# Performance work log

Measured on AMD Instinct MI355X. Metric: run time of the kernel, lower is better.

The kernel has to match this reference:

```python
import jax, jax.numpy as jnp
import numpy as np

INPUT_SIZE = 256
HIDDEN_SIZE = 256

def setup_inputs() -> dict:
    key = jax.random.key(0)
    ks = jax.random.split(key, 10)
    B = 65536
    scale_in = 1.0 / np.sqrt(INPUT_SIZE)
    scale_h = 1.0 / np.sqrt(HIDDEN_SIZE)
    inp = {
        "x": jax.random.normal(ks[0], (B, INPUT_SIZE), dtype=jnp.float32),
        "h_prev": jax.random.normal(ks[1], (B, HIDDEN_SIZE), dtype=jnp.float32),
        # nn.Linear weights are [out, in]; torch computes x @ W.T
        "W_z": jax.random.uniform(ks[2], (HIDDEN_SIZE, INPUT_SIZE), jnp.float32, -scale_in, scale_in),
        "U_z": jax.random.uniform(ks[3], (HIDDEN_SIZE, HIDDEN_SIZE), jnp.float32, -scale_h, scale_h),
        "b_z": jnp.zeros((HIDDEN_SIZE,), dtype=jnp.float32),
        "W_a": jax.random.uniform(ks[4], (HIDDEN_SIZE, INPUT_SIZE), jnp.float32, -scale_in, scale_in),
        "U_a": jax.random.uniform(ks[5], (HIDDEN_SIZE, HIDDEN_SIZE), jnp.float32, -scale_h, scale_h),
        "v_a": jax.random.normal(ks[6], (HIDDEN_SIZE,), dtype=jnp.float32),
        "W_h": jax.random.uniform(ks[7], (HIDDEN_SIZE, INPUT_SIZE), jnp.float32, -scale_in, scale_in),
        "U_h": jax.random.uniform(ks[8], (HIDDEN_SIZE, HIDDEN_SIZE), jnp.float32, -scale_h, scale_h),
        "b_h": jnp.zeros((HIDDEN_SIZE,), dtype=jnp.float32),
    }
    return inp

def reference(x, h_prev, W_z, U_z, b_z, W_a, U_a, v_a, W_h, U_h, b_h):
    # update gate
    z_t = jax.nn.sigmoid(x @ W_z.T + h_prev @ U_z.T + b_z)  # [B, H]
    # attention-based reset replacement
    attention_input = jnp.tanh(x @ W_a.T + h_prev @ U_a.T)   # [B, H]
    attention_weights = jax.nn.softmax(attention_input * v_a, axis=-1)
    attended_h = attention_weights * h_prev                   # [B, H]
    # candidate state
    h_tilde = jnp.tanh(x @ W_h.T + attended_h @ U_h.T + b_h)  # [B, H]
    # blend
    h_t = (1.0 - z_t) * h_prev + z_t * h_tilde
    return h_t
```

## Files before the change

### kernel.cpp

```cpp
#include <hip/hip_runtime.h>

typedef __attribute__((ext_vector_type(8))) short  short8v;
typedef __attribute__((ext_vector_type(4))) float  float4v;

#define BDIM 512

__device__ ushort g_w[3 * 8 * 2048 * 8];

__device__ __forceinline__ ushort f2bf(float f) {
  unsigned u = __float_as_uint(f);
  u += 0x7fffu + ((u >> 16) & 1u);
  return (ushort)(u >> 16);
}
__device__ __forceinline__ float bf2f(ushort s) {
  return __uint_as_float(((unsigned)s) << 16);
}

__global__ __launch_bounds__(256) void conv_w(
    const float* __restrict__ Wz, const float* __restrict__ Uz,
    const float* __restrict__ Wa, const float* __restrict__ Ua,
    const float* __restrict__ Wh, const float* __restrict__ Uh)
{
  int tid = blockIdx.x * 256 + threadIdx.x;
  int p  = tid >> 14;
  int rm = tid & 16383;
  int kb = rm >> 11;
  int n  = (rm >> 3) & 255;
  int c  = rm & 7;
  const float* W = (p == 0) ? Wz : (p == 1) ? Wa : Wh;
  const float* U = (p == 0) ? Uz : (p == 1) ? Ua : Uh;
  int k0 = kb * 64 + ((c ^ (n & 7)) << 3);
  const float* src = (k0 < 256) ? (W + n * 256 + k0) : (U + n * 256 + k0 - 256);
  uint pk[4];
#pragma unroll
  for (int jj = 0; jj < 4; ++jj) {
    float v0 = src[jj * 2], v1 = src[jj * 2 + 1];
    pk[jj] = (uint)f2bf(v0) | ((uint)f2bf(v1) << 16);
  }
  *reinterpret_cast<uint4*>(&g_w[(size_t)tid * 8]) = make_uint4(pk[0], pk[1], pk[2], pk[3]);
}

__global__ __launch_bounds__(BDIM, 2) void gru_fused(
    const float* __restrict__ x,  const float* __restrict__ hp,
    const float* __restrict__ bz, const float* __restrict__ va,
    const float* __restrict__ bh, float* __restrict__ out)
{
  __shared__ __align__(16) ushort sA[64 * 512];
  __shared__ __align__(16) ushort sB[2][256 * 64];
  __shared__ __align__(16) float  sRed[2][64 * 8];

  const int tid  = threadIdx.x;
  const int w    = tid >> 6;
  const int lane = tid & 63;
  const int g4   = lane >> 4;
  const int l15  = lane & 15;
  const int sxor = l15 & 7;
  const int rowBlk = blockIdx.x << 6;

  auto stageB = [&](int blkid, int buf) {
    const char* sb = (const char*)g_w + ((size_t)blkid << 15) + (w << 12) + (lane << 4);
    char* db = ((char*)&sB[buf][0]) + (w << 12);
#pragma unroll
    for (int i = 0; i < 4; ++i) {
      __builtin_amdgcn_global_load_lds(
          (const __attribute__((address_space(1))) void*)(sb + i * 1024),
          (__attribute__((address_space(3))) void*)(db + i * 1024),
          16, 0, 0);
    }
  };

  stageB(0, 0);

  {
    const float4* xq = reinterpret_cast<const float4*>(x)  + (size_t)rowBlk * 64;
    const float4* hq = reinterpret_cast<const float4*>(hp) + (size_t)rowBlk * 64;
#pragma unroll
    for (int i = 0; i < 16; ++i) {
      int q   = tid + i * BDIM;
      int row = q >> 7;
      int qc  = q & 127;
      float4 v = (qc < 64) ? xq[row * 64 + qc] : hq[row * 64 + qc - 64];
      int kE  = qc << 2;
      int swz = (kE >> 3) ^ (row & 7);
      ushort4 pk4;
      pk4.x = f2bf(v.x); pk4.y = f2bf(v.y); pk4.z = f2bf(v.z); pk4.w = f2bf(v.w);
      *reinterpret_cast<ushort4*>((char*)sA + (row << 10) + (swz << 4) + ((kE & 7) << 1)) = pk4;
    }
  }
  __syncthreads();

  float4v acc[4][2];
  float   zf[4][2][4];
  float   hv[4][2][4];
  int cur = 0;

  for (int p = 0; p < 3; ++p) {
#pragma unroll
    for (int m = 0; m < 4; ++m)
#pragma unroll
      for (int r = 0; r < 2; ++r)
        acc[m][r] = (float4v){0.f, 0.f, 0.f, 0.f};

    for (int kb = 0; kb < 8; ++kb) {
      int blk = p * 8 + kb;
      if (blk < 23) stageB(blk + 1, cur ^ 1);

      short8v afr[2][4], bfr[2][2];
#pragma unroll
      for (int s = 0; s < 2; ++s) {
#pragma unroll
        for (int m = 0; m < 4; ++m) {
          int row = m * 16 + l15;
          int swz = (kb * 8 + s * 4 + g4) ^ sxor;
          afr[s][m] = *reinterpret_cast<const short8v*>((const char*)sA + (row << 10) + (swz << 4));
        }
#pragma unroll
        for (int r = 0; r < 2; ++r) {
          int n   = (w << 5) + (r << 4) + l15;
          int swz = (s * 4 + g4) ^ sxor;
          bfr[s][r] = *reinterpret_cast<const short8v*>((const char*)&sB[cur][0] + (n << 7) + (swz << 4));
        }
      }
#pragma unroll
      for (int s = 0; s < 2; ++s)
#pragma unroll
        for (int m = 0; m < 4; ++m)
#pragma unroll
          for (int r = 0; r < 2; ++r)
            acc[m][r] = __builtin_amdgcn_mfma_f32_16x16x32_bf16(afr[s][m], bfr[s][r], acc[m][r], 0, 0, 0);

      __syncthreads();
      cur ^= 1;
    }

    if (p == 0) {
#pragma unroll
      for (int r = 0; r < 2; ++r) {
        float b = bz[(w << 5) + (r << 4) + l15];
#pragma unroll
        for (int m = 0; m < 4; ++m)
#pragma unroll
          for (int j = 0; j < 4; ++j)
            zf[m][r][j] = 1.f / (1.f + __expf(-(acc[m][r][j] + b)));
      }
    } else if (p == 1) {
      float vav[2];
      vav[0] = va[(w << 5) + l15];
      vav[1] = va[(w << 5) + 16 + l15];
#pragma unroll
      for (int m = 0; m < 4; ++m)
#pragma unroll
        for (int r = 0; r < 2; ++r)
#pragma unroll
          for (int j = 0; j < 4; ++j) {
            float s = acc[m][r][j];
            float t = 1.f - 2.f / (__expf(2.f * s) + 1.f);
            acc[m][r][j] = t * vav[r];
          }
      float mx[4][4];
#pragma unroll
      for (int m = 0; m < 4; ++m)
#pragma unroll
        for (int j = 0; j < 4; ++j) {
          float v = fmaxf(acc[m][0][j], acc[m][1][j]);
          v = fmaxf(v, __shfl_xor(v, 1));
          v = fmaxf(v, __shfl_xor(v, 2));
          v = fmaxf(v, __shfl_xor(v, 4));
          v = fmaxf(v, __shfl_xor(v, 8));
          mx[m][j] = v;
        }
      if (l15 == 0) {
#pragma unroll
        for (int m = 0; m < 4; ++m)
#pragma unroll
          for (int j = 0; j < 4; ++j)
            sRed[0][((m * 16 + g4 * 4 + j) << 3) + w] = mx[m][j];
      }
      __syncthreads();
      float rmax[4][4], rsum[4][4];
#pragma unroll
      for (int m = 0; m < 4; ++m)
#pragma unroll
        for (int j = 0; j < 4; ++j) {
          int row = m * 16 + g4 * 4 + j;
          const float4* pr = reinterpret_cast<const float4*>(&sRed[0][row << 3]);
          float4 a = pr[0], b = pr[1];
          rmax[m][j] = fmaxf(fmaxf(fmaxf(a.x, a.y), fmaxf(a.z, a.w)),
                             fmaxf(fmaxf(b.x, b.y), fmaxf(b.z, b.w)));
        }
#pragma unroll
      for (int m = 0; m < 4; ++m)
#pragma unroll
        for (int j = 0; j < 4; ++j) {
          float e0 = __expf(acc[m][0][j] - rmax[m][j]);
          float e1 = __expf(acc[m][1][j] - rmax[m][j]);
          acc[m][0][j] = e0; acc[m][1][j] = e1;
          float sm = e0 + e1;
          sm += __shfl_xor(sm, 1);
          sm += __shfl_xor(sm, 2);
          sm += __shfl_xor(sm, 4);
          sm += __shfl_xor(sm, 8);
          rsum[m][j] = sm;
        }
      if (l15 == 0) {
#pragma unroll
        for (int m = 0; m < 4; ++m)
#pragma unroll
          for (int j = 0; j < 4; ++j)
            sRed[1][((m * 16 + g4 * 4 + j) << 3) + w] = rsum[m][j];
      }
#pragma unroll
      for (int m = 0; m < 4; ++m)
#pragma unroll
        for (int r = 0; r < 2; ++r)
#pragma unroll
          for (int j = 0; j < 4; ++j) {
            int row = m * 16 + g4 * 4 + j;
            int cs  = (32 + (w << 2) + (r << 1) + (l15 >> 3)) ^ (row & 7);
            hv[m][r][j] = bf2f(sA[(row << 9) + (cs << 3) + sxor]);
          }
      __syncthreads();
#pragma unroll
      for (int m = 0; m < 4; ++m)
#pragma unroll
        for (int j = 0; j < 4; ++j) {
          int row = m * 16 + g4 * 4 + j;
          const float4* pr = reinterpret_cast<const float4*>(&sRed[1][row << 3]);
          float4 a = pr[0], b = pr[1];
          float s = (a.x + a.y) + (a.z + a.w) + (b.x + b.y) + (b.z + b.w);
          float inv = 1.f / s;
#pragma unroll
          for (int r = 0; r < 2; ++r) {
            float at = acc[m][r][j] * inv * hv[m][r][j];
            int cs = (32 + (w << 2) + (r << 1) + (l15 >> 3)) ^ (row & 7);
            sA[(row << 9) + (cs << 3) + sxor] = f2bf(at);
          }
        }
      __syncthreads();
    } else {
#pragma unroll
      for (int r = 0; r < 2; ++r) {
        float b = bh[(w << 5) + (r << 4) + l15];
#pragma unroll
        for (int m = 0; m < 4; ++m)
#pragma unroll
          for (int j = 0; j < 4; ++j) {
            float s  = acc[m][r][j] + b;
            float ht = 1.f - 2.f / (__expf(2.f * s) + 1.f);
            float z  = zf[m][r][j];
            float res = (1.f - z) * hv[m][r][j] + z * ht;
            int row = m * 16 + g4 * 4 + j;
            out[(size_t)(rowBlk + row) * 256 + (w << 5) + (r << 4) + l15] = res;
          }
      }
    }
  }
}

extern "C" void kernel_launch(void* const* d_in, const int* in_sizes, int n_in,
                              void* d_out, int out_size, void* d_ws, size_t ws_size,
                              hipStream_t stream)
{
  const float* x  = (const float*)d_in[0];
  const float* hp = (const float*)d_in[1];
  const float* Wz = (const float*)d_in[2];
  const float* Uz = (const float*)d_in[3];
  const float* bz = (const float*)d_in[4];
  const float* Wa = (const float*)d_in[5];
  const float* Ua = (const float*)d_in[6];
  const float* va = (const float*)d_in[7];
  const float* Wh = (const float*)d_in[8];
  const float* Uh = (const float*)d_in[9];
  const float* bh = (const float*)d_in[10];
  float* out = (float*)d_out;

  conv_w<<<dim3(192), dim3(256), 0, stream>>>(Wz, Uz, Wa, Ua, Wh, Uh);
  gru_fused<<<dim3(1024), dim3(BDIM), 0, stream>>>(x, hp, bz, va, bh, out);
}
```

Baseline: 370.2 us.

## Load weight fragments directly into registers instead of LDS staging

Reorders the precomputed bf16 weight buffer into MFMA fragment order so each wave reads its B operands straight from global memory into registers. Even and odd register sets double-buffer the loads, and the per-k-block barrier and LDS weight buffer go away. The h_prev values needed at the end are moved from registers into a shared array so fewer registers stay live across the three GEMM phases. The cost is more global or L2 traffic per wave, since weights are no longer shared through LDS across the block, and the global load latency is now exposed within each k-step.

Measured after the change: 407.5 us. 10.1% more time.

```diff
diff --git a/kernel.cpp b/kernel.cpp
--- a/kernel.cpp
+++ b/kernel.cpp
@@ -5,7 +5,7 @@
 
 #define BDIM 512
 
-__device__ ushort g_w[3 * 8 * 2048 * 8];
+__device__ ushort g_w[3 * 8 * 16 * 2 * 64 * 8];
 
 __device__ __forceinline__ ushort f2bf(float f) {
   unsigned u = __float_as_uint(f);
@@ -22,15 +22,16 @@
     const float* __restrict__ Wh, const float* __restrict__ Uh)
 {
   int tid = blockIdx.x * 256 + threadIdx.x;
-  int p  = tid >> 14;
-  int rm = tid & 16383;
-  int kb = rm >> 11;
-  int n  = (rm >> 3) & 255;
-  int c  = rm & 7;
+  int p   = tid >> 14;
+  int kb  = (tid >> 11) & 7;
+  int c16 = (tid >> 7) & 15;
+  int s   = (tid >> 6) & 1;
+  int l   = tid & 63;
   const float* W = (p == 0) ? Wz : (p == 1) ? Wa : Wh;
   const float* U = (p == 0) ? Uz : (p == 1) ? Ua : Uh;
-  int k0 = kb * 64 + ((c ^ (n & 7)) << 3);
-  const float* src = (k0 < 256) ? (W + n * 256 + k0) : (U + n * 256 + k0 - 256);
+  int col = c16 * 16 + (l & 15);
+  int k0  = kb * 64 + s * 32 + ((l >> 4) << 3);
+  const float* src = (k0 < 256) ? (W + col * 256 + k0) : (U + col * 256 + (k0 - 256));
   uint pk[4];
 #pragma unroll
   for (int jj = 0; jj < 4; ++jj) {
@@ -46,7 +47,7 @@
     const float* __restrict__ bh, float* __restrict__ out)
 {
   __shared__ __align__(16) ushort sA[64 * 512];
-  __shared__ __align__(16) ushort sB[2][256 * 64];
+  __shared__ __align__(16) ushort sHv[64 * 256];
   __shared__ __align__(16) float  sRed[2][64 * 8];
 
   const int tid  = threadIdx.x;
@@ -57,19 +58,18 @@
   const int sxor = l15 & 7;
   const int rowBlk = blockIdx.x << 6;
 
-  auto stageB = [&](int blkid, int buf) {
-    const char* sb = (const char*)g_w + ((size_t)blkid << 15) + (w << 12) + (lane << 4);
-    char* db = ((char*)&sB[buf][0]) + (w << 12);
-#pragma unroll
-    for (int i = 0; i < 4; ++i) {
-      __builtin_amdgcn_global_load_lds(
-          (const __attribute__((address_space(1))) void*)(sb + i * 1024),
-          (__attribute__((address_space(3))) void*)(db + i * 1024),
-          16, 0, 0);
-    }
+  const ushort* wbase = g_w + (size_t)(w * 2048) + (size_t)lane * 8;
+  short8v bEven[2][2], bOdd[2][2];
+  auto loadB = [&](int blk, short8v (&b)[2][2]) {
+    const ushort* pb = wbase + (size_t)blk * 16384;
+#pragma unroll
+    for (int s = 0; s < 2; ++s)
+#pragma unroll
+      for (int r = 0; r < 2; ++r)
+        b[s][r] = *reinterpret_cast<const short8v*>(pb + r * 1024 + s * 512);
   };
 
-  stageB(0, 0);
+  loadB(0, bEven);
 
   {
     const float4* xq = reinterpret_cast<const float4*>(x)  + (size_t)rowBlk * 64;
@@ -91,8 +91,6 @@
 
   float4v acc[4][2];
   float   zf[4][2][4];
-  float   hv[4][2][4];
-  int cur = 0;
 
   for (int p = 0; p < 3; ++p) {
 #pragma unroll
@@ -101,36 +99,30 @@
       for (int r = 0; r < 2; ++r)
         acc[m][r] = (float4v){0.f, 0.f, 0.f, 0.f};
 
+#pragma unroll
     for (int kb = 0; kb < 8; ++kb) {
-      int blk = p * 8 + kb;
-      if (blk < 23) stageB(blk + 1, cur ^ 1);
-
-      short8v afr[2][4], bfr[2][2];
-#pragma unroll
-      for (int s = 0; s < 2; ++s) {
+      const int blk = p * 8 + kb;
+      if (blk < 23) {
+        if (kb & 1) loadB(blk + 1, bEven);
+        else        loadB(blk + 1, bOdd);
+      }
+      short8v afr[2][4];
+#pragma unroll
+      for (int s = 0; s < 2; ++s)
 #pragma unroll
         for (int m = 0; m < 4; ++m) {
           int row = m * 16 + l15;
           int swz = (kb * 8 + s * 4 + g4) ^ sxor;
           afr[s][m] = *reinterpret_cast<const short8v*>((const char*)sA + (row << 10) + (swz << 4));
         }
-#pragma unroll
-        for (int r = 0; r < 2; ++r) {
-          int n   = (w << 5) + (r << 4) + l15;
-          int swz = (s * 4 + g4) ^ sxor;
-          bfr[s][r] = *reinterpret_cast<const short8v*>((const char*)&sB[cur][0] + (n << 7) + (swz << 4));
-        }
-      }
+      const short8v (&bC)[2][2] = (kb & 1) ? bOdd : bEven;
 #pragma unroll
       for (int s = 0; s < 2; ++s)
 #pragma unroll
         for (int m = 0; m < 4; ++m)
 #pragma unroll
           for (int r = 0; r < 2; ++r)
-            acc[m][r] = __builtin_amdgcn_mfma_f32_16x16x32_bf16(afr[s][m], bfr[s][r], acc[m][r], 0, 0, 0);
-
-      __syncthreads();
-      cur ^= 1;
+            acc[m][r] = __builtin_amdgcn_mfma_f32_16x16x32_bf16(afr[s][m], bC[s][r], acc[m][r], 0, 0, 0);
     }
 
     if (p == 0) {
@@ -177,7 +169,7 @@
             sRed[0][((m * 16 + g4 * 4 + j) << 3) + w] = mx[m][j];
       }
       __syncthreads();
-      float rmax[4][4], rsum[4][4];
+      float rmax[4][4];
 #pragma unroll
       for (int m = 0; m < 4; ++m)
 #pragma unroll
@@ -200,15 +192,9 @@
           sm += __shfl_xor(sm, 2);
           sm += __shfl_xor(sm, 4);
           sm += __shfl_xor(sm, 8);
-          rsum[m][j] = sm;
-        }
-      if (l15 == 0) {
-#pragma unroll
-        for (int m = 0; m < 4; ++m)
-#pragma unroll
-          for (int j = 0; j < 4; ++j)
-            sRed[1][((m * 16 + g4 * 4 + j) << 3) + w] = rsum[m][j];
-      }
+          if (l15 == 0) sRed[1][((m * 16 + g4 * 4 + j) << 3) + w] = sm;
+        }
+      float hv[4][2][4];
 #pragma unroll
       for (int m = 0; m < 4; ++m)
 #pragma unroll
@@ -231,9 +217,11 @@
           float inv = 1.f / s;
 #pragma unroll
           for (int r = 0; r < 2; ++r) {
-            float at = acc[m][r][j] * inv * hv[m][r][j];
+            float hval = hv[m][r][j];
+            float at = acc[m][r][j] * inv * hval;
             int cs = (32 + (w << 2) + (r << 1) + (l15 >> 3)) ^ (row & 7);
             sA[(row << 9) + (cs << 3) + sxor] = f2bf(at);
+            sHv[row * 256 + (w << 5) + (r << 4) + l15] = f2bf(hval);
           }
         }
       __syncthreads();
@@ -248,8 +236,9 @@
             float s  = acc[m][r][j] + b;
             float ht = 1.f - 2.f / (__expf(2.f * s) + 1.f);
             float z  = zf[m][r][j];
-            float res = (1.f - z) * hv[m][r][j] + z * ht;
             int row = m * 16 + g4 * 4 + j;
+            float h0 = bf2f(sHv[row * 256 + (w << 5) + (r << 4) + l15]);
+            float res = (1.f - z) * h0 + z * ht;
             out[(size_t)(rowBlk + row) * 256 + (w << 5) + (r << 4) + l15] = res;
           }
       }
```
